# Optimization experiments

Measured on AMD Instinct MI355X. Metric: run time of the kernel, lower is better.

Reference implementation:

```python
import jax, jax.numpy as jnp
import numpy as np

D_IN = 1024
D_OUT = 1024
NUM_HEADS = 16
HEAD_DIM = D_OUT // NUM_HEADS


def setup_inputs() -> dict:
    key = jax.random.key(0)
    ks = jax.random.split(key, 6)
    s = 0.02
    x = jax.random.normal(ks[0], (2, 2048, D_IN), dtype=jnp.float32)
    Wq = jax.random.normal(ks[1], (D_IN, D_OUT), dtype=jnp.float32) * s
    Wk = jax.random.normal(ks[2], (D_IN, D_OUT), dtype=jnp.float32) * s
    Wv = jax.random.normal(ks[3], (D_IN, D_OUT), dtype=jnp.float32) * s
    Wo = jax.random.normal(ks[4], (D_OUT, D_OUT), dtype=jnp.float32) * s
    bo = jnp.zeros((D_OUT,), dtype=jnp.float32)
    return {"x": x, "Wq": Wq, "Wk": Wk, "Wv": Wv, "Wo": Wo, "bo": bo}


def reference(x, Wq, Wk, Wv, Wo, bo):
    b, n, _ = x.shape
    # project and split heads: [b, h, n, d]
    def heads(W):
        return (x @ W).reshape(b, n, NUM_HEADS, HEAD_DIM).transpose(0, 2, 1, 3)
    q, k, v = heads(Wq), heads(Wk), heads(Wv)
    scores = jnp.einsum("bhqd,bhkd->bhqk", q, k)  # [b,h,n,n]
    causal = jnp.tril(jnp.ones((n, n), dtype=bool))  # True = keep
    scores = jnp.where(causal, scores, -jnp.inf)
    attn = jax.nn.softmax(scores / np.sqrt(HEAD_DIM).astype(np.float32), axis=-1)
    ctx = jnp.einsum("bhqk,bhkd->bhqd", attn, v)
    ctx = ctx.transpose(0, 2, 1, 3).reshape(b, n, D_OUT)
    return ctx @ Wo + bo
```

## Files before the change

### kernel.cpp

```cpp
#include <hip/hip_runtime.h>
#include <stdint.h>

typedef unsigned short u16;
typedef __attribute__((ext_vector_type(8))) __bf16 bf16x8;
typedef __attribute__((ext_vector_type(4))) float f32x4;
typedef __attribute__((ext_vector_type(16))) float f32x16;

#define D_IN 1024
#define NH 16
#define DH 64
#define BATCH 2
#define SEQ 2048

#define QSCL 0.1803368801111244f

#define GLD_LDS16(gp, lp)                                                              \
  __builtin_amdgcn_global_load_lds((__attribute__((address_space(1))) const void*)(gp), \
                                   (__attribute__((address_space(3))) void*)(lp), 16, 0, 0)

__device__ __forceinline__ u16 f2b(float f) {
  union { float ff; uint32_t u; } v; v.ff = f;
  return (u16)((v.u + 0x7fffu + ((v.u >> 16) & 1u)) >> 16);
}

__device__ __forceinline__ float swap32f(float v) { return __shfl_xor(v, 32, 64); }

__device__ __forceinline__ uint32_t cvtpk(float a, float b) {
  uint32_t r;
  asm("v_cvt_pk_bf16_f32 %0, %1, %2" : "=v"(r) : "v"(a), "v"(b));
  return r;
}
__device__ __forceinline__ float fexp2(float x) {
  float r;
  asm("v_exp_f32 %0, %1" : "=v"(r) : "v"(x));
  return r;
}

__global__ __launch_bounds__(256)
void prep_kernel(const float* __restrict__ x, u16* __restrict__ xb,
                 const float* __restrict__ W0, const float* __restrict__ W1,
                 const float* __restrict__ W2, const float* __restrict__ W3,
                 u16* __restrict__ T0, u16* __restrict__ T1,
                 u16* __restrict__ T2, u16* __restrict__ T3) {
  __shared__ float tile[32][33];
  if (blockIdx.x < 4096) {
    const int i = (blockIdx.x * 256 + threadIdx.x) * 4;
    const float4 v = *(const float4*)(x + i);
    uint2 pack;
    pack.x = (uint32_t)f2b(v.x) | ((uint32_t)f2b(v.y) << 16);
    pack.y = (uint32_t)f2b(v.z) | ((uint32_t)f2b(v.w) << 16);
    *(uint2*)(xb + i) = pack;
  } else {
    const int bid2 = blockIdx.x - 4096;
    const float* W; u16* T;
    switch (bid2 >> 10) {
      case 0: W = W0; T = T0; break;
      case 1: W = W1; T = T1; break;
      case 2: W = W2; T = T2; break;
      default: W = W3; T = T3; break;
    }
    const int rem = bid2 & 1023;
    const int n0 = (rem >> 5) * 32, k0 = (rem & 31) * 32;
    const int tx = threadIdx.x & 31, ty = threadIdx.x >> 5;
    #pragma unroll
    for (int i = 0; i < 32; i += 8)
      tile[ty + i][tx] = W[(size_t)(k0 + ty + i) * D_IN + n0 + tx];
    __syncthreads();
    #pragma unroll
    for (int i = 0; i < 32; i += 8)
      T[(size_t)(n0 + ty + i) * D_IN + k0 + tx] = f2b(tile[tx][ty + i]);
  }
}

__global__ __launch_bounds__(256)
void gemm_qkv_kernel(const u16* __restrict__ Xb,
                     const u16* __restrict__ WqT, const u16* __restrict__ WkT,
                     const u16* __restrict__ WvT,
                     u16* __restrict__ Qo, u16* __restrict__ Ko, u16* __restrict__ Vt) {
  __shared__ u16 As[128 * 32];
  __shared__ u16 Bs[128 * 32];
  const int which = blockIdx.z;
  const u16* Bt = (which == 0) ? WqT : (which == 1) ? WkT : WvT;

  const int tid = threadIdx.x;
  const int lane = tid & 63;
  const int w = tid >> 6;
  const int bm = blockIdx.x * 128;
  const int bn = blockIdx.y * 128;
  const int wr = w >> 1, wc = w & 1;
  const int g = lane >> 4, lm = lane & 15;
  const int srow = lane >> 2;
  const int scol = (lane & 3) * 8;

  const f32x4 zero = {0.f, 0.f, 0.f, 0.f};
  f32x4 acc[4][4];
  #pragma unroll
  for (int i = 0; i < 4; ++i)
    #pragma unroll
    for (int n = 0; n < 4; ++n) acc[i][n] = zero;

  for (int k0 = 0; k0 < D_IN; k0 += 32) {
    __syncthreads();
    #pragma unroll
    for (int L = 0; L < 2; ++L) {
      const int chunk = w * 2 + L;
      const int r = chunk * 16 + srow;
      GLD_LDS16(Xb + (size_t)(bm + r) * D_IN + k0 + scol, As + chunk * 512);
      GLD_LDS16(Bt + (size_t)(bn + r) * D_IN + k0 + scol, Bs + chunk * 512);
    }
    __syncthreads();

    bf16x8 af[4], bf[4];
    #pragma unroll
    for (int i = 0; i < 4; ++i)
      af[i] = *(const bf16x8*)(As + (wr * 64 + i * 16 + lm) * 32 + g * 8);
    #pragma unroll
    for (int n = 0; n < 4; ++n)
      bf[n] = *(const bf16x8*)(Bs + (wc * 64 + n * 16 + lm) * 32 + g * 8);
    #pragma unroll
    for (int i = 0; i < 4; ++i)
      #pragma unroll
      for (int n = 0; n < 4; ++n)
        acc[i][n] = __builtin_amdgcn_mfma_f32_16x16x32_bf16(af[i], bf[n], acc[i][n], 0, 0, 0);
  }

  const float oscale = (which == 0) ? QSCL : 1.0f;
  #pragma unroll
  for (int i = 0; i < 4; ++i) {
    #pragma unroll
    for (int n = 0; n < 4; ++n) {
      #pragma unroll
      for (int r = 0; r < 4; ++r) {
        const int m = bm + wr * 64 + i * 16 + g * 4 + r;
        const int c = bn + wc * 64 + n * 16 + lm;
        const int b = m >> 11, nn = m & (SEQ - 1);
        const int h = c >> 6, d = c & (DH - 1);
        const int bh = b * NH + h;
        const int t = nn >> 5;
        const u16 val = f2b(acc[i][n][r] * oscale);
        if (which == 2) {
          const int n5 = nn & 31;
          const int f = (n5 >> 4) * 2 + (d >> 5);
          const int lane2 = ((n5 >> 2) & 1) * 32 + (d & 31);
          const int j = ((n5 >> 3) & 1) * 4 + (n5 & 3);
          Vt[((size_t)(bh * 64 + t) * 4 + f) * 512 + lane2 * 8 + j] = val;
        } else {
          const int st = d >> 4;
          const int lane2 = ((d >> 3) & 1) * 32 + (nn & 31);
          const int j = d & 7;
          const size_t idx = ((size_t)(bh * 64 + t) * 4 + st) * 512 + lane2 * 8 + j;
          if (which == 0) Qo[idx] = val; else Ko[idx] = val;
        }
      }
    }
  }
}

__global__ __launch_bounds__(256)
void attn4_kernel(const u16* __restrict__ Qb, const u16* __restrict__ Kb,
                  const u16* __restrict__ Vt, u16* __restrict__ Ctx) {
  __shared__ float mbuf[4][32][64];
  __shared__ float lbuf[4][32];

  const int tid = threadIdx.x;
  const int lane = tid & 63;
  const int kw = tid >> 6;
  const int ql = lane & 31;
  const int hi = lane >> 5;
  const int bid = blockIdx.x;
  const int c = bid & 7;
  const int r = bid >> 3;
  const int jj = r & 31;
  const int bh = c + 8 * (r >> 5);
  const int b = bh >> 4, h = bh & 15;

  const u16* Qf = Qb + (size_t)bh * 64 * 2048;
  const u16* Kf = Kb + (size_t)bh * 64 * 2048;
  const u16* Vf = Vt + (size_t)bh * 64 * 2048;
  const int lofs = lane * 8;

  #pragma unroll 1
  for (int pass = 0; pass < 2; ++pass) {
    const int qt = pass ? (63 - jj) : jj;
    const int qb0 = qt * 32;

    bf16x8 qf[4];
    {
      const u16* qp = Qf + (size_t)qt * 2048 + lofs;
      #pragma unroll
      for (int st = 0; st < 4; ++st) qf[st] = *(const bf16x8*)(qp + st * 512);
    }

    f32x16 ctx0 = {0,0,0,0,0,0,0,0,0,0,0,0,0,0,0,0};
    f32x16 ctx1 = {0,0,0,0,0,0,0,0,0,0,0,0,0,0,0,0};
    float lacc[4] = {0.f, 0.f, 0.f, 0.f};

    bf16x8 kf[4], vf[4];
    if (kw <= qt) {
      {
        const u16* kp = Kf + (size_t)kw * 2048 + lofs;
        const u16* vp = Vf + (size_t)kw * 2048 + lofs;
        #pragma unroll
        for (int st = 0; st < 4; ++st) kf[st] = *(const bf16x8*)(kp + st * 512);
        #pragma unroll
        for (int f = 0; f < 4; ++f) vf[f] = *(const bf16x8*)(vp + f * 512);
      }
      #pragma unroll 1
      for (int t = kw; t <= qt; t += 4) {
        f32x16 s = {0,0,0,0,0,0,0,0,0,0,0,0,0,0,0,0};
        #pragma unroll
        for (int st = 0; st < 4; ++st)
          s = __builtin_amdgcn_mfma_f32_32x32x16_bf16(kf[st], qf[st], s, 0, 0, 0);

        const int tn = (t + 4 <= qt) ? (t + 4) : qt;
        {
          const u16* kp = Kf + (size_t)tn * 2048 + lofs;
          #pragma unroll
          for (int st = 0; st < 4; ++st) kf[st] = *(const bf16x8*)(kp + st * 512);
        }

        float p[16];
        if (t == qt) {
          #pragma unroll
          for (int cr = 0; cr < 16; ++cr) {
            const int kl = ((cr & 3) + 8 * (cr >> 2)) + 4 * hi;
            p[cr] = (kl > ql) ? 0.f : fexp2(s[cr]);
          }
        } else {
          #pragma unroll
          for (int cr = 0; cr < 16; ++cr) p[cr] = fexp2(s[cr]);
        }
        #pragma unroll
        for (int cr = 0; cr < 16; ++cr) lacc[cr & 3] += p[cr];

        #pragma unroll
        for (int ks = 0; ks < 2; ++ks) {
          uint4 pw;
          pw.x = cvtpk(p[ks * 8 + 0], p[ks * 8 + 1]);
          pw.y = cvtpk(p[ks * 8 + 2], p[ks * 8 + 3]);
          pw.z = cvtpk(p[ks * 8 + 4], p[ks * 8 + 5]);
          pw.w = cvtpk(p[ks * 8 + 6], p[ks * 8 + 7]);
          union { uint4 u; bf16x8 v; } pa; pa.u = pw;
          ctx0 = __builtin_amdgcn_mfma_f32_32x32x16_bf16(vf[ks * 2 + 0], pa.v, ctx0, 0, 0, 0);
          ctx1 = __builtin_amdgcn_mfma_f32_32x32x16_bf16(vf[ks * 2 + 1], pa.v, ctx1, 0, 0, 0);
        }

        {
          const u16* vp = Vf + (size_t)tn * 2048 + lofs;
          #pragma unroll
          for (int f = 0; f < 4; ++f) vf[f] = *(const bf16x8*)(vp + f * 512);
        }
      }
    }

    const float lloc = (lacc[0] + lacc[1]) + (lacc[2] + lacc[3]);
    const float lwv = lloc + swap32f(lloc);

    #pragma unroll
    for (int grp = 0; grp < 4; ++grp) {
      const int ch = grp * 2 + hi;
      f32x4 t0 = {ctx0[grp * 4 + 0], ctx0[grp * 4 + 1], ctx0[grp * 4 + 2], ctx0[grp * 4 + 3]};
      f32x4 t1 = {ctx1[grp * 4 + 0], ctx1[grp * 4 + 1], ctx1[grp * 4 + 2], ctx1[grp * 4 + 3]};
      *(f32x4*)&mbuf[kw][ql][(ch ^ ql) * 4 & 63]       = t0;
      *(f32x4*)&mbuf[kw][ql][((ch + 8) ^ ql) * 4 & 63] = t1;
    }
    if (lane < 32) lbuf[kw][ql] = lwv;
    __syncthreads();

    {
      const int ch0 = kw * 4 + hi * 2;
      f32x4 a0 = {0.f, 0.f, 0.f, 0.f}, a1 = {0.f, 0.f, 0.f, 0.f};
      #pragma unroll
      for (int p2 = 0; p2 < 4; ++p2) {
        a0 += *(const f32x4*)&mbuf[p2][ql][(ch0 ^ ql) * 4 & 63];
        a1 += *(const f32x4*)&mbuf[p2][ql][((ch0 + 1) ^ ql) * 4 & 63];
      }
      const float lt = (lbuf[0][ql] + lbuf[1][ql]) + (lbuf[2][ql] + lbuf[3][ql]);
      const float inv = __builtin_amdgcn_rcpf(lt);
      uint4 pw;
      pw.x = cvtpk(a0[0] * inv, a0[1] * inv);
      pw.y = cvtpk(a0[2] * inv, a0[3] * inv);
      pw.z = cvtpk(a1[0] * inv, a1[1] * inv);
      pw.w = cvtpk(a1[2] * inv, a1[3] * inv);
      *(uint4*)(Ctx + (size_t)(b * SEQ + qb0 + ql) * 1024 + h * 64 + kw * 16 + hi * 8) = pw;
    }
    __syncthreads();
  }
}

__global__ __launch_bounds__(256)
void gemm_out_kernel(const u16* __restrict__ Ctx, const u16* __restrict__ WoT,
                     const float* __restrict__ bo, float* __restrict__ out) {
  __shared__ u16 As[128 * 32];
  __shared__ u16 Bs[128 * 32];
  const int tid = threadIdx.x;
  const int lane = tid & 63;
  const int w = tid >> 6;
  const int bm = blockIdx.x * 128;
  const int bn = blockIdx.y * 128;
  const int wr = w >> 1, wc = w & 1;
  const int g = lane >> 4, lm = lane & 15;
  const int srow = lane >> 2;
  const int scol = (lane & 3) * 8;

  const f32x4 zero = {0.f, 0.f, 0.f, 0.f};
  f32x4 acc[4][4];
  #pragma unroll
  for (int i = 0; i < 4; ++i)
    #pragma unroll
    for (int n = 0; n < 4; ++n) acc[i][n] = zero;

  for (int k0 = 0; k0 < D_IN; k0 += 32) {
    __syncthreads();
    #pragma unroll
    for (int L = 0; L < 2; ++L) {
      const int chunk = w * 2 + L;
      const int r = chunk * 16 + srow;
      GLD_LDS16(Ctx + (size_t)(bm + r) * D_IN + k0 + scol, As + chunk * 512);
      GLD_LDS16(WoT + (size_t)(bn + r) * D_IN + k0 + scol, Bs + chunk * 512);
    }
    __syncthreads();

    bf16x8 af[4], bf[4];
    #pragma unroll
    for (int i = 0; i < 4; ++i)
      af[i] = *(const bf16x8*)(As + (wr * 64 + i * 16 + lm) * 32 + g * 8);
    #pragma unroll
    for (int n = 0; n < 4; ++n)
      bf[n] = *(const bf16x8*)(Bs + (wc * 64 + n * 16 + lm) * 32 + g * 8);
    #pragma unroll
    for (int i = 0; i < 4; ++i)
      #pragma unroll
      for (int n = 0; n < 4; ++n)
        acc[i][n] = __builtin_amdgcn_mfma_f32_16x16x32_bf16(af[i], bf[n], acc[i][n], 0, 0, 0);
  }

  #pragma unroll
  for (int i = 0; i < 4; ++i)
    #pragma unroll
    for (int n = 0; n < 4; ++n)
      #pragma unroll
      for (int r = 0; r < 4; ++r) {
        const int m = bm + wr * 64 + i * 16 + g * 4 + r;
        const int cidx = bn + wc * 64 + n * 16 + lm;
        out[(size_t)m * 1024 + cidx] = acc[i][n][r] + bo[cidx];
      }
}

extern "C" void kernel_launch(void* const* d_in, const int* in_sizes, int n_in,
                              void* d_out, int out_size, void* d_ws, size_t ws_size,
                              hipStream_t stream) {
  (void)in_sizes; (void)n_in; (void)out_size; (void)ws_size;
  const float* x  = (const float*)d_in[0];
  const float* Wq = (const float*)d_in[1];
  const float* Wk = (const float*)d_in[2];
  const float* Wv = (const float*)d_in[3];
  const float* Wo = (const float*)d_in[4];
  const float* bo = (const float*)d_in[5];
  float* out = (float*)d_out;

  char* ws = (char*)d_ws;
  u16* xb  = (u16*)(ws);
  u16* WqT = (u16*)(ws + (8u << 20));
  u16* WkT = (u16*)(ws + (10u << 20));
  u16* WvT = (u16*)(ws + (12u << 20));
  u16* WoT = (u16*)(ws + (14u << 20));
  u16* Qb  = (u16*)(ws + (16u << 20));
  u16* Kb  = (u16*)(ws + (24u << 20));
  u16* Vt  = (u16*)(ws + (32u << 20));
  u16* Ctx = xb;

  prep_kernel<<<dim3(8192), 256, 0, stream>>>(x, xb, Wq, Wk, Wv, Wo, WqT, WkT, WvT, WoT);
  gemm_qkv_kernel<<<dim3(32, 8, 3), 256, 0, stream>>>(xb, WqT, WkT, WvT, Qb, Kb, Vt);
  attn4_kernel<<<dim3(1024), 256, 0, stream>>>(Qb, Kb, Vt, Ctx);
  gemm_out_kernel<<<dim3(32, 8), 256, 0, stream>>>(Ctx, WoT, bo, out);
}
```

Measured before the change: 103.4 us.

## Double-buffer LDS tiles in QKV and output GEMMs to overlap loads with MFMA

Both projection GEMMs now keep two LDS buffers per operand. The global-to-LDS loads for the next K-slice are issued before the MFMAs on the current slice run. This leaves one barrier per iteration instead of two and hides global load latency behind compute. The cost is double the LDS footprint per block, which may reduce occupancy, plus a manual vmcnt wait and barrier protocol.

```diff
diff --git a/kernel.cpp b/kernel.cpp
--- a/kernel.cpp
+++ b/kernel.cpp
@@ -77,8 +77,8 @@
                      const u16* __restrict__ WqT, const u16* __restrict__ WkT,
                      const u16* __restrict__ WvT,
                      u16* __restrict__ Qo, u16* __restrict__ Ko, u16* __restrict__ Vt) {
-  __shared__ u16 As[128 * 32];
-  __shared__ u16 Bs[128 * 32];
+  __shared__ u16 As[2][128 * 32];
+  __shared__ u16 Bs[2][128 * 32];
   const int which = blockIdx.z;
   const u16* Bt = (which == 0) ? WqT : (which == 1) ? WkT : WvT;
 
@@ -91,6 +91,8 @@
   const int g = lane >> 4, lm = lane & 15;
   const int srow = lane >> 2;
   const int scol = (lane & 3) * 8;
+  const int chunk0 = w * 2, chunk1 = w * 2 + 1;
+  const int r0 = chunk0 * 16 + srow, r1 = chunk1 * 16 + srow;
 
   const f32x4 zero = {0.f, 0.f, 0.f, 0.f};
   f32x4 acc[4][4];
@@ -99,30 +101,40 @@
     #pragma unroll
     for (int n = 0; n < 4; ++n) acc[i][n] = zero;
 
-  for (int k0 = 0; k0 < D_IN; k0 += 32) {
-    __syncthreads();
-    #pragma unroll
-    for (int L = 0; L < 2; ++L) {
-      const int chunk = w * 2 + L;
-      const int r = chunk * 16 + srow;
-      GLD_LDS16(Xb + (size_t)(bm + r) * D_IN + k0 + scol, As + chunk * 512);
-      GLD_LDS16(Bt + (size_t)(bn + r) * D_IN + k0 + scol, Bs + chunk * 512);
-    }
-    __syncthreads();
-
+  auto stage = [&](int buf, int k0) {
+    GLD_LDS16(Xb + (size_t)(bm + r0) * D_IN + k0 + scol, &As[buf][chunk0 * 512]);
+    GLD_LDS16(Bt + (size_t)(bn + r0) * D_IN + k0 + scol, &Bs[buf][chunk0 * 512]);
+    GLD_LDS16(Xb + (size_t)(bm + r1) * D_IN + k0 + scol, &As[buf][chunk1 * 512]);
+    GLD_LDS16(Bt + (size_t)(bn + r1) * D_IN + k0 + scol, &Bs[buf][chunk1 * 512]);
+  };
+  auto compute = [&](int buf) {
     bf16x8 af[4], bf[4];
     #pragma unroll
     for (int i = 0; i < 4; ++i)
-      af[i] = *(const bf16x8*)(As + (wr * 64 + i * 16 + lm) * 32 + g * 8);
+      af[i] = *(const bf16x8*)(&As[buf][(wr * 64 + i * 16 + lm) * 32 + g * 8]);
     #pragma unroll
     for (int n = 0; n < 4; ++n)
-      bf[n] = *(const bf16x8*)(Bs + (wc * 64 + n * 16 + lm) * 32 + g * 8);
+      bf[n] = *(const bf16x8*)(&Bs[buf][(wc * 64 + n * 16 + lm) * 32 + g * 8]);
     #pragma unroll
     for (int i = 0; i < 4; ++i)
       #pragma unroll
       for (int n = 0; n < 4; ++n)
         acc[i][n] = __builtin_amdgcn_mfma_f32_16x16x32_bf16(af[i], bf[n], acc[i][n], 0, 0, 0);
+  };
+
+  stage(0, 0);
+  asm volatile("s_waitcnt vmcnt(0)" ::: "memory");
+  __builtin_amdgcn_s_barrier();
+  int cur = 0;
+  #pragma unroll 1
+  for (int t = 0; t < 31; ++t) {
+    stage(cur ^ 1, (t + 1) * 32);
+    compute(cur);
+    asm volatile("s_waitcnt vmcnt(0)" ::: "memory");
+    __builtin_amdgcn_s_barrier();
+    cur ^= 1;
   }
+  compute(cur);
 
   const float oscale = (which == 0) ? QSCL : 1.0f;
   #pragma unroll
@@ -291,8 +303,8 @@
 __global__ __launch_bounds__(256)
 void gemm_out_kernel(const u16* __restrict__ Ctx, const u16* __restrict__ WoT,
                      const float* __restrict__ bo, float* __restrict__ out) {
-  __shared__ u16 As[128 * 32];
-  __shared__ u16 Bs[128 * 32];
+  __shared__ u16 As[2][128 * 32];
+  __shared__ u16 Bs[2][128 * 32];
   const int tid = threadIdx.x;
   const int lane = tid & 63;
   const int w = tid >> 6;
@@ -302,6 +314,8 @@
   const int g = lane >> 4, lm = lane & 15;
   const int srow = lane >> 2;
   const int scol = (lane & 3) * 8;
+  const int chunk0 = w * 2, chunk1 = w * 2 + 1;
+  const int r0 = chunk0 * 16 + srow, r1 = chunk1 * 16 + srow;
 
   const f32x4 zero = {0.f, 0.f, 0.f, 0.f};
   f32x4 acc[4][4];
@@ -310,30 +324,40 @@
     #pragma unroll
     for (int n = 0; n < 4; ++n) acc[i][n] = zero;
 
-  for (int k0 = 0; k0 < D_IN; k0 += 32) {
-    __syncthreads();
-    #pragma unroll
-    for (int L = 0; L < 2; ++L) {
-      const int chunk = w * 2 + L;
-      const int r = chunk * 16 + srow;
-      GLD_LDS16(Ctx + (size_t)(bm + r) * D_IN + k0 + scol, As + chunk * 512);
-      GLD_LDS16(WoT + (size_t)(bn + r) * D_IN + k0 + scol, Bs + chunk * 512);
-    }
-    __syncthreads();
-
+  auto stage = [&](int buf, int k0) {
+    GLD_LDS16(Ctx + (size_t)(bm + r0) * D_IN + k0 + scol, &As[buf][chunk0 * 512]);
+    GLD_LDS16(WoT + (size_t)(bn + r0) * D_IN + k0 + scol, &Bs[buf][chunk0 * 512]);
+    GLD_LDS16(Ctx + (size_t)(bm + r1) * D_IN + k0 + scol, &As[buf][chunk1 * 512]);
+    GLD_LDS16(WoT + (size_t)(bn + r1) * D_IN + k0 + scol, &Bs[buf][chunk1 * 512]);
+  };
+  auto compute = [&](int buf) {
     bf16x8 af[4], bf[4];
     #pragma unroll
     for (int i = 0; i < 4; ++i)
-      af[i] = *(const bf16x8*)(As + (wr * 64 + i * 16 + lm) * 32 + g * 8);
+      af[i] = *(const bf16x8*)(&As[buf][(wr * 64 + i * 16 + lm) * 32 + g * 8]);
     #pragma unroll
     for (int n = 0; n < 4; ++n)
-      bf[n] = *(const bf16x8*)(Bs + (wc * 64 + n * 16 + lm) * 32 + g * 8);
+      bf[n] = *(const bf16x8*)(&Bs[buf][(wc * 64 + n * 16 + lm) * 32 + g * 8]);
     #pragma unroll
     for (int i = 0; i < 4; ++i)
       #pragma unroll
       for (int n = 0; n < 4; ++n)
         acc[i][n] = __builtin_amdgcn_mfma_f32_16x16x32_bf16(af[i], bf[n], acc[i][n], 0, 0, 0);
+  };
+
+  stage(0, 0);
+  asm volatile("s_waitcnt vmcnt(0)" ::: "memory");
+  __builtin_amdgcn_s_barrier();
+  int cur = 0;
+  #pragma unroll 1
+  for (int t = 0; t < 31; ++t) {
+    stage(cur ^ 1, (t + 1) * 32);
+    compute(cur);
+    asm volatile("s_waitcnt vmcnt(0)" ::: "memory");
+    __builtin_amdgcn_s_barrier();
+    cur ^= 1;
   }
+  compute(cur);
 
   #pragma unroll
   for (int i = 0; i < 4; ++i)
```

Result: slower. 113.4 us (+9.7%).

## Double-buffer GEMM K-tiles with XOR-swizzled LDS and fuse Q/K/V projections into one kernel

Applied to the files above, without the earlier changes.

Both GEMM kernels now use 64-wide K tiles, double-buffered in LDS with asynchronous global-to-LDS loads, and an XOR swizzle on the LDS layout to avoid bank conflicts. The QKV GEMM is merged into a single 512-thread block that computes Q, K and V for the same X tile, so X is loaded once instead of three times. The attention inner loop is unrolled by two. The cost is more LDS per block (about 128KB for QKV) and fewer blocks in flight, which lowers occupancy.

```diff
diff --git a/kernel.cpp b/kernel.cpp
--- a/kernel.cpp
+++ b/kernel.cpp
@@ -72,84 +72,145 @@
   }
 }
 
-__global__ __launch_bounds__(256)
+__device__ __forceinline__ void qkv_compute(
+    const u16* __restrict__ AsB, const u16* __restrict__ Bq,
+    const u16* __restrict__ Bk, const u16* __restrict__ Bv,
+    int wm, int wn, int g, int lm,
+    f32x4 accq[4][2], f32x4 acck[4][2], f32x4 accv[4][2]) {
+  #pragma unroll
+  for (int kk = 0; kk < 2; ++kk) {
+    const int slot = ((kk * 4 + g) ^ (lm & 7)) << 3;
+    bf16x8 af[4];
+    #pragma unroll
+    for (int i = 0; i < 4; ++i)
+      af[i] = *(const bf16x8*)(AsB + (wm * 64 + i * 16 + lm) * 64 + slot);
+    bf16x8 bq[2], bk[2], bv[2];
+    #pragma unroll
+    for (int n = 0; n < 2; ++n) {
+      const int ro = (wn * 32 + n * 16 + lm) * 64 + slot;
+      bq[n] = *(const bf16x8*)(Bq + ro);
+      bk[n] = *(const bf16x8*)(Bk + ro);
+      bv[n] = *(const bf16x8*)(Bv + ro);
+    }
+    #pragma unroll
+    for (int i = 0; i < 4; ++i)
+      #pragma unroll
+      for (int n = 0; n < 2; ++n) {
+        accq[i][n] = __builtin_amdgcn_mfma_f32_16x16x32_bf16(af[i], bq[n], accq[i][n], 0, 0, 0);
+        acck[i][n] = __builtin_amdgcn_mfma_f32_16x16x32_bf16(af[i], bk[n], acck[i][n], 0, 0, 0);
+        accv[i][n] = __builtin_amdgcn_mfma_f32_16x16x32_bf16(af[i], bv[n], accv[i][n], 0, 0, 0);
+      }
+  }
+}
+
+__global__ __launch_bounds__(512)
 void gemm_qkv_kernel(const u16* __restrict__ Xb,
                      const u16* __restrict__ WqT, const u16* __restrict__ WkT,
                      const u16* __restrict__ WvT,
                      u16* __restrict__ Qo, u16* __restrict__ Ko, u16* __restrict__ Vt) {
-  __shared__ u16 As[128 * 32];
-  __shared__ u16 Bs[128 * 32];
-  const int which = blockIdx.z;
-  const u16* Bt = (which == 0) ? WqT : (which == 1) ? WkT : WvT;
+  __shared__ u16 As[2][128 * 64];
+  __shared__ u16 Bs[2][3][128 * 64];
 
   const int tid = threadIdx.x;
   const int lane = tid & 63;
   const int w = tid >> 6;
+  const int wm = w >> 2, wn = w & 3;
   const int bm = blockIdx.x * 128;
   const int bn = blockIdx.y * 128;
-  const int wr = w >> 1, wc = w & 1;
   const int g = lane >> 4, lm = lane & 15;
-  const int srow = lane >> 2;
-  const int scol = (lane & 3) * 8;
-
-  const f32x4 zero = {0.f, 0.f, 0.f, 0.f};
-  f32x4 acc[4][4];
+
+  const int r_in = lane >> 3;
+  const int s_w = lane & 7;
+  const int swz_col = (s_w ^ r_in) << 3;
+
+  const int c0 = w * 2;
+  const u16* a_src0 = Xb + (size_t)(bm + c0 * 8 + r_in) * D_IN + swz_col;
+  const u16* a_src1 = a_src0 + 8 * D_IN;
+  const u16* q_src0 = WqT + (size_t)(bn + c0 * 8 + r_in) * D_IN + swz_col;
+  const u16* q_src1 = q_src0 + 8 * D_IN;
+  const u16* k_src0 = WkT + (size_t)(bn + c0 * 8 + r_in) * D_IN + swz_col;
+  const u16* k_src1 = k_src0 + 8 * D_IN;
+  const u16* v_src0 = WvT + (size_t)(bn + c0 * 8 + r_in) * D_IN + swz_col;
+  const u16* v_src1 = v_src0 + 8 * D_IN;
+
+#define QKV_STAGE(BUF, K0)                                 \
+  do {                                                     \
+    GLD_LDS16(a_src0 + (K0), &As[BUF][c0 * 512]);          \
+    GLD_LDS16(a_src1 + (K0), &As[BUF][c0 * 512 + 512]);    \
+    GLD_LDS16(q_src0 + (K0), &Bs[BUF][0][c0 * 512]);       \
+    GLD_LDS16(q_src1 + (K0), &Bs[BUF][0][c0 * 512 + 512]); \
+    GLD_LDS16(k_src0 + (K0), &Bs[BUF][1][c0 * 512]);       \
+    GLD_LDS16(k_src1 + (K0), &Bs[BUF][1][c0 * 512 + 512]); \
+    GLD_LDS16(v_src0 + (K0), &Bs[BUF][2][c0 * 512]);       \
+    GLD_LDS16(v_src1 + (K0), &Bs[BUF][2][c0 * 512 + 512]); \
+  } while (0)
+
+  f32x4 accq[4][2], acck[4][2], accv[4][2];
   #pragma unroll
   for (int i = 0; i < 4; ++i)
     #pragma unroll
-    for (int n = 0; n < 4; ++n) acc[i][n] = zero;
-
-  for (int k0 = 0; k0 < D_IN; k0 += 32) {
-    __syncthreads();
-    #pragma unroll
-    for (int L = 0; L < 2; ++L) {
-      const int chunk = w * 2 + L;
-      const int r = chunk * 16 + srow;
-      GLD_LDS16(Xb + (size_t)(bm + r) * D_IN + k0 + scol, As + chunk * 512);
-      GLD_LDS16(Bt + (size_t)(bn + r) * D_IN + k0 + scol, Bs + chunk * 512);
-    }
-    __syncthreads();
-
-    bf16x8 af[4], bf[4];
-    #pragma unroll
-    for (int i = 0; i < 4; ++i)
-      af[i] = *(const bf16x8*)(As + (wr * 64 + i * 16 + lm) * 32 + g * 8);
-    #pragma unroll
-    for (int n = 0; n < 4; ++n)
-      bf[n] = *(const bf16x8*)(Bs + (wc * 64 + n * 16 + lm) * 32 + g * 8);
-    #pragma unroll
-    for (int i = 0; i < 4; ++i)
-      #pragma unroll
-      for (int n = 0; n < 4; ++n)
-        acc[i][n] = __builtin_amdgcn_mfma_f32_16x16x32_bf16(af[i], bf[n], acc[i][n], 0, 0, 0);
-  }
-
-  const float oscale = (which == 0) ? QSCL : 1.0f;
+    for (int n = 0; n < 2; ++n) {
+      accq[i][n] = {0.f, 0.f, 0.f, 0.f};
+      acck[i][n] = {0.f, 0.f, 0.f, 0.f};
+      accv[i][n] = {0.f, 0.f, 0.f, 0.f};
+    }
+
+  QKV_STAGE(0, 0);
+  QKV_STAGE(1, 64);
+  #pragma unroll 1
+  for (int tt = 0; tt < 7; ++tt) {
+    asm volatile("s_waitcnt vmcnt(8)" ::: "memory");
+    __builtin_amdgcn_s_barrier();
+    qkv_compute(As[0], Bs[0][0], Bs[0][1], Bs[0][2], wm, wn, g, lm, accq, acck, accv);
+    __builtin_amdgcn_s_barrier();
+    QKV_STAGE(0, (2 * tt + 2) * 64);
+    asm volatile("s_waitcnt vmcnt(8)" ::: "memory");
+    __builtin_amdgcn_s_barrier();
+    qkv_compute(As[1], Bs[1][0], Bs[1][1], Bs[1][2], wm, wn, g, lm, accq, acck, accv);
+    __builtin_amdgcn_s_barrier();
+    QKV_STAGE(1, (2 * tt + 3) * 64);
+  }
+  asm volatile("s_waitcnt vmcnt(8)" ::: "memory");
+  __builtin_amdgcn_s_barrier();
+  qkv_compute(As[0], Bs[0][0], Bs[0][1], Bs[0][2], wm, wn, g, lm, accq, acck, accv);
+  asm volatile("s_waitcnt vmcnt(0)" ::: "memory");
+  __builtin_amdgcn_s_barrier();
+  qkv_compute(As[1], Bs[1][0], Bs[1][1], Bs[1][2], wm, wn, g, lm, accq, acck, accv);
+#undef QKV_STAGE
+
   #pragma unroll
   for (int i = 0; i < 4; ++i) {
     #pragma unroll
-    for (int n = 0; n < 4; ++n) {
+    for (int n = 0; n < 2; ++n) {
       #pragma unroll
       for (int r = 0; r < 4; ++r) {
-        const int m = bm + wr * 64 + i * 16 + g * 4 + r;
-        const int c = bn + wc * 64 + n * 16 + lm;
+        const int m = bm + wm * 64 + i * 16 + g * 4 + r;
+        const int c = bn + wn * 32 + n * 16 + lm;
         const int b = m >> 11, nn = m & (SEQ - 1);
         const int h = c >> 6, d = c & (DH - 1);
         const int bh = b * NH + h;
         const int t = nn >> 5;
-        const u16 val = f2b(acc[i][n][r] * oscale);
-        if (which == 2) {
+        {
+          const u16 val = f2b(accq[i][n][r] * QSCL);
+          const int st = d >> 4;
+          const int lane2 = ((d >> 3) & 1) * 32 + (nn & 31);
+          const int j = d & 7;
+          Qo[((size_t)(bh * 64 + t) * 4 + st) * 512 + lane2 * 8 + j] = val;
+        }
+        {
+          const u16 val = f2b(acck[i][n][r]);
+          const int st = d >> 4;
+          const int lane2 = ((d >> 3) & 1) * 32 + (nn & 31);
+          const int j = d & 7;
+          Ko[((size_t)(bh * 64 + t) * 4 + st) * 512 + lane2 * 8 + j] = val;
+        }
+        {
+          const u16 val = f2b(accv[i][n][r]);
           const int n5 = nn & 31;
           const int f = (n5 >> 4) * 2 + (d >> 5);
           const int lane2 = ((n5 >> 2) & 1) * 32 + (d & 31);
           const int j = ((n5 >> 3) & 1) * 4 + (n5 & 3);
           Vt[((size_t)(bh * 64 + t) * 4 + f) * 512 + lane2 * 8 + j] = val;
-        } else {
-          const int st = d >> 4;
-          const int lane2 = ((d >> 3) & 1) * 32 + (nn & 31);
-          const int j = d & 7;
-          const size_t idx = ((size_t)(bh * 64 + t) * 4 + st) * 512 + lane2 * 8 + j;
-          if (which == 0) Qo[idx] = val; else Ko[idx] = val;
         }
       }
     }
@@ -205,7 +266,7 @@
         #pragma unroll
         for (int f = 0; f < 4; ++f) vf[f] = *(const bf16x8*)(vp + f * 512);
       }
-      #pragma unroll 1
+      #pragma unroll 2
       for (int t = kw; t <= qt; t += 4) {
         f32x16 s = {0,0,0,0,0,0,0,0,0,0,0,0,0,0,0,0};
         #pragma unroll
@@ -288,11 +349,32 @@
   }
 }
 
+__device__ __forceinline__ void out_compute(
+    const u16* __restrict__ AsB, const u16* __restrict__ BsB,
+    int wr, int wc, int g, int lm, f32x4 acc[4][4]) {
+  #pragma unroll
+  for (int kk = 0; kk < 2; ++kk) {
+    const int slot = ((kk * 4 + g) ^ (lm & 7)) << 3;
+    bf16x8 af[4], bf[4];
+    #pragma unroll
+    for (int i = 0; i < 4; ++i)
+      af[i] = *(const bf16x8*)(AsB + (wr * 64 + i * 16 + lm) * 64 + slot);
+    #pragma unroll
+    for (int n = 0; n < 4; ++n)
+      bf[n] = *(const bf16x8*)(BsB + (wc * 64 + n * 16 + lm) * 64 + slot);
+    #pragma unroll
+    for (int i = 0; i < 4; ++i)
+      #pragma unroll
+      for (int n = 0; n < 4; ++n)
+        acc[i][n] = __builtin_amdgcn_mfma_f32_16x16x32_bf16(af[i], bf[n], acc[i][n], 0, 0, 0);
+  }
+}
+
 __global__ __launch_bounds__(256)
 void gemm_out_kernel(const u16* __restrict__ Ctx, const u16* __restrict__ WoT,
                      const float* __restrict__ bo, float* __restrict__ out) {
-  __shared__ u16 As[128 * 32];
-  __shared__ u16 Bs[128 * 32];
+  __shared__ u16 As[2][128 * 64];
+  __shared__ u16 Bs[2][128 * 64];
   const int tid = threadIdx.x;
   const int lane = tid & 63;
   const int w = tid >> 6;
@@ -300,40 +382,52 @@
   const int bn = blockIdx.y * 128;
   const int wr = w >> 1, wc = w & 1;
   const int g = lane >> 4, lm = lane & 15;
-  const int srow = lane >> 2;
-  const int scol = (lane & 3) * 8;
-
-  const f32x4 zero = {0.f, 0.f, 0.f, 0.f};
+
+  const int r_in = lane >> 3;
+  const int s_w = lane & 7;
+  const int swz_col = (s_w ^ r_in) << 3;
+
+  const int c0 = w * 4;
+  const u16* a_src = Ctx + (size_t)(bm + c0 * 8 + r_in) * D_IN + swz_col;
+  const u16* b_src = WoT + (size_t)(bn + c0 * 8 + r_in) * D_IN + swz_col;
+
+#define OUT_STAGE(BUF, K0)                                             \
+  do {                                                                 \
+    _Pragma("unroll")                                                  \
+    for (int j = 0; j < 4; ++j) {                                      \
+      GLD_LDS16(a_src + j * 8 * D_IN + (K0), &As[BUF][(c0 + j) * 512]); \
+      GLD_LDS16(b_src + j * 8 * D_IN + (K0), &Bs[BUF][(c0 + j) * 512]); \
+    }                                                                  \
+  } while (0)
+
   f32x4 acc[4][4];
   #pragma unroll
   for (int i = 0; i < 4; ++i)
     #pragma unroll
-    for (int n = 0; n < 4; ++n) acc[i][n] = zero;
-
-  for (int k0 = 0; k0 < D_IN; k0 += 32) {
-    __syncthreads();
-    #pragma unroll
-    for (int L = 0; L < 2; ++L) {
-      const int chunk = w * 2 + L;
-      const int r = chunk * 16 + srow;
-      GLD_LDS16(Ctx + (size_t)(bm + r) * D_IN + k0 + scol, As + chunk * 512);
-      GLD_LDS16(WoT + (size_t)(bn + r) * D_IN + k0 + scol, Bs + chunk * 512);
-    }
-    __syncthreads();
-
-    bf16x8 af[4], bf[4];
-    #pragma unroll
-    for (int i = 0; i < 4; ++i)
-      af[i] = *(const bf16x8*)(As + (wr * 64 + i * 16 + lm) * 32 + g * 8);
-    #pragma unroll
-    for (int n = 0; n < 4; ++n)
-      bf[n] = *(const bf16x8*)(Bs + (wc * 64 + n * 16 + lm) * 32 + g * 8);
-    #pragma unroll
-    for (int i = 0; i < 4; ++i)
-      #pragma unroll
-      for (int n = 0; n < 4; ++n)
-        acc[i][n] = __builtin_amdgcn_mfma_f32_16x16x32_bf16(af[i], bf[n], acc[i][n], 0, 0, 0);
-  }
+    for (int n = 0; n < 4; ++n) acc[i][n] = {0.f, 0.f, 0.f, 0.f};
+
+  OUT_STAGE(0, 0);
+  OUT_STAGE(1, 64);
+  #pragma unroll 1
+  for (int tt = 0; tt < 7; ++tt) {
+    asm volatile("s_waitcnt vmcnt(8)" ::: "memory");
+    __builtin_amdgcn_s_barrier();
+    out_compute(As[0], Bs[0], wr, wc, g, lm, acc);
+    __builtin_amdgcn_s_barrier();
+    OUT_STAGE(0, (2 * tt + 2) * 64);
+    asm volatile("s_waitcnt vmcnt(8)" ::: "memory");
+    __builtin_amdgcn_s_barrier();
+    out_compute(As[1], Bs[1], wr, wc, g, lm, acc);
+    __builtin_amdgcn_s_barrier();
+    OUT_STAGE(1, (2 * tt + 3) * 64);
+  }
+  asm volatile("s_waitcnt vmcnt(8)" ::: "memory");
+  __builtin_amdgcn_s_barrier();
+  out_compute(As[0], Bs[0], wr, wc, g, lm, acc);
+  asm volatile("s_waitcnt vmcnt(0)" ::: "memory");
+  __builtin_amdgcn_s_barrier();
+  out_compute(As[1], Bs[1], wr, wc, g, lm, acc);
+#undef OUT_STAGE
 
   #pragma unroll
   for (int i = 0; i < 4; ++i)
@@ -371,7 +465,7 @@
   u16* Ctx = xb;
 
   prep_kernel<<<dim3(8192), 256, 0, stream>>>(x, xb, Wq, Wk, Wv, Wo, WqT, WkT, WvT, WoT);
-  gemm_qkv_kernel<<<dim3(32, 8, 3), 256, 0, stream>>>(xb, WqT, WkT, WvT, Qb, Kb, Vt);
+  gemm_qkv_kernel<<<dim3(32, 8), 512, 0, stream>>>(xb, WqT, WkT, WvT, Qb, Kb, Vt);
   attn4_kernel<<<dim3(1024), 256, 0, stream>>>(Qb, Kb, Vt, Ctx);
   gemm_out_kernel<<<dim3(32, 8), 256, 0, stream>>>(Ctx, WoT, bo, out);
 }
```

Result: faster. 92.65 us (-10.4%).
